# Kernel optimization log

Hardware: AMD Instinct MI355X
Metric: run time of the kernel (lower is better)

Reference implementation:

```python
import jax, jax.numpy as jnp
import numpy as np

IM_H, IM_W = 32, 32
HEADS, HEAD_DIM = 8, 32
IN_DIM = 256
OUT_DIM = 256
N = IM_H * IM_W


def _relative_indices(h, w):
    # replicate torch meshgrid('ij') + flatten logic
    gy, gx = np.meshgrid(np.arange(h), np.arange(w), indexing='ij')
    pos = np.stack([gy.reshape(-1), gx.reshape(-1)])  # (2, n)
    rel = pos[:, :, None] - pos[:, None, :]           # (2, n, n)
    r0 = (rel[0] + (h - 1)) * (2 * w - 1)
    r1 = rel[1] + (w - 1)
    return (r0 + r1).reshape(-1)                      # (n*n,)

_REL_IDX = jnp.asarray(_relative_indices(IM_H, IM_W), dtype=jnp.int32)


def setup_inputs() -> dict:
    key = jax.random.key(0)
    ks = jax.random.split(key, 8)
    d_inner = HEADS * HEAD_DIM
    x = jax.random.normal(ks[0], (16, N, IN_DIM), dtype=jnp.float32)
    Wq = jax.random.normal(ks[1], (IN_DIM, d_inner), dtype=jnp.float32) / np.sqrt(IN_DIM)
    Wk = jax.random.normal(ks[2], (IN_DIM, d_inner), dtype=jnp.float32) / np.sqrt(IN_DIM)
    Wv = jax.random.normal(ks[3], (IN_DIM, d_inner), dtype=jnp.float32) / np.sqrt(IN_DIM)
    bias_table = jax.random.normal(ks[4], ((2 * IM_H - 1) * (2 * IM_W - 1), HEADS), dtype=jnp.float32)
    Wo = jax.random.normal(ks[5], (d_inner, OUT_DIM), dtype=jnp.float32) / np.sqrt(d_inner)
    bo = jax.random.normal(ks[6], (OUT_DIM,), dtype=jnp.float32) * 0.01
    return {"x": x, "Wq": Wq, "Wk": Wk, "Wv": Wv, "bias_table": bias_table, "Wo": Wo, "bo": bo}


def reference(x, Wq, Wk, Wv, bias_table, Wo, bo):
    b, n, _ = x.shape
    scale = HEAD_DIM ** (-0.5)
    # QKV projections -> [b, h, n, d]
    def proj(W):
        return (x @ W).reshape(b, n, HEADS, HEAD_DIM).transpose(0, 2, 1, 3)
    Q, K, V = proj(Wq), proj(Wk), proj(Wv)
    # gathered relative position bias -> [1, h, n, n]
    bias = bias_table[_REL_IDX].reshape(n, n, HEADS).transpose(2, 0, 1)[None]
    scores = jnp.einsum('bhnd,bhmd->bhnm', Q, K) * scale + bias
    attn = jax.nn.softmax(scores, axis=-1)
    out = jnp.einsum('bhnm,bhmd->bhnd', attn, V)
    out = out.transpose(0, 2, 1, 3).reshape(b, n, HEADS * HEAD_DIM)
    return out @ Wo + bo  # dropout is identity in eval mode
```

## Files before the change

kernel.cpp:

```cpp
#include <hip/hip_runtime.h>


using f32x4  = __attribute__((ext_vector_type(4))) float;
using bf16x8 = __attribute__((ext_vector_type(8))) short;

__device__ __forceinline__ short f2bf(float f) {
  union { float f; unsigned u; } v; v.f = f;
  return (short)((v.u + 0x7FFFu + ((v.u >> 16) & 1u)) >> 16);
}
__device__ __forceinline__ f32x4 mfma_k32(bf16x8 a, bf16x8 b, f32x4 c) {
  return __builtin_amdgcn_mfma_f32_16x16x32_bf16(a, b, c, 0, 0, 0);
}
__device__ __forceinline__ int cvt_pk_bf16(float lo, float hi) {
  int r;
  asm("v_cvt_pk_bf16_f32 %0, %1, %2" : "=v"(r) : "v"(lo), "v"(hi));
  return r;
}
__device__ __forceinline__ f32x4 ldb(const float* __restrict__ row, int p) {
  f32x4 v;
  v[0] = row[p]; v[1] = row[p - 1]; v[2] = row[p - 2]; v[3] = row[p - 3];
  return v;
}

#define CSQ 0.25500526817f

__global__ __launch_bounds__(256) void k_prep(const float* __restrict__ Wq,
    const float* __restrict__ Wk, const float* __restrict__ Wv,
    const float* __restrict__ Wo, short* __restrict__ WT,
    const float* __restrict__ bt, float* __restrict__ Tg) {
  int bx = blockIdx.x;
  if (bx < 64) {
    __shared__ float tile[64][65];
    int wid = bx >> 4, t = bx & 15;
    int ro0 = (t & 3) * 64, co0 = (t >> 2) * 64;
    const float* W = wid == 0 ? Wq : wid == 1 ? Wk : wid == 2 ? Wv : Wo;
    int tr = threadIdx.x >> 4, tc = threadIdx.x & 15;
    #pragma unroll
    for (int c = 0; c < 4; ++c) {
      int row = c * 16 + tr;
      float4 v = *reinterpret_cast<const float4*>(
          &W[(ro0 + row) * 256 + co0 + tc * 4]);
      tile[row][tc * 4 + 0] = v.x;
      tile[row][tc * 4 + 1] = v.y;
      tile[row][tc * 4 + 2] = v.z;
      tile[row][tc * 4 + 3] = v.w;
    }
    __syncthreads();
    #pragma unroll
    for (int c = 0; c < 4; ++c) {
      int orow = c * 16 + tr;
      short4 s;
      s.x = f2bf(tile[tc * 4 + 0][orow]);
      s.y = f2bf(tile[tc * 4 + 1][orow]);
      s.z = f2bf(tile[tc * 4 + 2][orow]);
      s.w = f2bf(tile[tc * 4 + 3][orow]);
      *reinterpret_cast<short4*>(
          &WT[wid * 65536 + (co0 + orow) * 256 + ro0 + tc * 4]) = s;
    }
  } else {
    int idx = (bx - 64) * 256 + threadIdx.x;
    int h = idx >> 12, i = idx & 4095;
    if (i < 3969) Tg[idx] = bt[i * 8 + h] * 1.4426950408889634f;
  }
}

__global__ __launch_bounds__(256) void k_qkv(const float* __restrict__ x,
    const short* __restrict__ WT,
    short* __restrict__ Q, short* __restrict__ K, short* __restrict__ Vt) {
  __shared__ short Wlds[2][4096];
  char* lbase = (char*)Wlds;
  const int tid = threadIdx.x;
  const int w = tid >> 6, l = tid & 63, lr = l & 15, lg = l >> 4;
  const int m0 = blockIdx.x * 64;
  const int wi = blockIdx.y;
  const char* Wb = (const char*)(WT + wi * 65536);
  const float* xrow = x + (size_t)(m0 + w * 16 + lr) * 256;
  bf16x8 af[8];
  #pragma unroll
  for (int kc = 0; kc < 8; ++kc) {
    float4 a = *reinterpret_cast<const float4*>(xrow + kc * 32 + lg * 8);
    float4 c = *reinterpret_cast<const float4*>(xrow + kc * 32 + lg * 8 + 4);
    union { int i4[4]; bf16x8 v; } u;
    u.i4[0] = cvt_pk_bf16(a.x, a.y);
    u.i4[1] = cvt_pk_bf16(a.z, a.w);
    u.i4[2] = cvt_pk_bf16(c.x, c.y);
    u.i4[3] = cvt_pk_bf16(c.z, c.w);
    af[kc] = u.v;
  }
  const int Lb0 = tid * 16, Lb1 = 4096 + tid * 16;
  const int P0 = Lb0 ^ (((Lb0 >> 9) & 7) << 4);
  const int P1 = Lb1 ^ (((Lb1 >> 9) & 7) << 4);
  int rdo[8];
  #pragma unroll
  for (int kc = 0; kc < 8; ++kc) {
    int Lg = lr * 512 + kc * 64 + lg * 16;
    rdo[kc] = Lg ^ ((lr & 7) << 4);
  }
  {
    int4 s0 = *reinterpret_cast<const int4*>(Wb + Lb0);
    int4 s1 = *reinterpret_cast<const int4*>(Wb + Lb1);
    *reinterpret_cast<int4*>(lbase + P0) = s0;
    *reinterpret_cast<int4*>(lbase + P1) = s1;
  }
  __syncthreads();
  #pragma unroll 2
  for (int nt = 0; nt < 16; ++nt) {
    const int cur = nt & 1, nxt = cur ^ 1;
    int4 t0, t1;
    if (nt < 15) {
      t0 = *reinterpret_cast<const int4*>(Wb + (nt + 1) * 8192 + Lb0);
      t1 = *reinterpret_cast<const int4*>(Wb + (nt + 1) * 8192 + Lb1);
    }
    f32x4 acc = {0.f, 0.f, 0.f, 0.f};
    #pragma unroll
    for (int kc = 0; kc < 8; ++kc) {
      bf16x8 bfr = *reinterpret_cast<const bf16x8*>(lbase + cur * 8192 + rdo[kc]);
      acc = mfma_k32(af[kc], bfr, acc);
    }
    int colb = nt * 16 + lr;
    int h = colb >> 5, d = colb & 31;
    if (wi == 2) {
      int m = m0 + w * 16 + lg * 4;
      int b = m >> 10, n0 = m & 1023;
      int js = n0 >> 5;
      int lgv = (n0 & 15) >> 2, hi = (n0 >> 4) & 1;
      int jp = lgv * 8 + hi * 4;
      short4 vv;
      vv.x = f2bf(acc[0]); vv.y = f2bf(acc[1]);
      vv.z = f2bf(acc[2]); vv.w = f2bf(acc[3]);
      *reinterpret_cast<short4*>(
          &Vt[(((size_t)(b * 8 + h) * 32 + js) << 10) + d * 32 + jp]) = vv;
    } else {
      #pragma unroll
      for (int r = 0; r < 4; ++r) {
        int m = m0 + w * 16 + lg * 4 + r;
        int b = m >> 10, n = m & 1023;
        short val = (wi == 0) ? f2bf(acc[r] * CSQ) : f2bf(acc[r]);
        if (wi == 0)
          Q[((size_t)(b * 8 + h) * 1024 + n) * 32 + d] = val;
        else
          K[((size_t)(b * 8 + h) * 1024 + n) * 32 + d] = val;
      }
    }
    if (nt < 15) {
      *reinterpret_cast<int4*>(lbase + nxt * 8192 + P0) = t0;
      *reinterpret_cast<int4*>(lbase + nxt * 8192 + P1) = t1;
    }
    __syncthreads();
  }
}

__global__ __launch_bounds__(512) void k_attn(const short* __restrict__ Q,
    const short* __restrict__ K, const short* __restrict__ Vt,
    const float* __restrict__ Tg, short* __restrict__ aout) {
  __shared__ char smraw[24576];
  float* Tlds = (float*)smraw;
  auto mO  = (float(*)[4][4][64])smraw;
  auto mls = (float(*)[2][4][64])(smraw + 16384);
  const int tid = threadIdx.x, bid = blockIdx.x;
  const int h = bid & 7, qt = (bid >> 3) & 7, b = bid >> 6;
  const float* Th = Tg + (h << 12);
  for (int t = tid; t < 3969; t += 512) Tlds[t] = Th[t];
  __syncthreads();
  const int wg = tid >> 6, l = tid & 63, lr = l & 15, lg = l >> 4;
  const int w = wg & 3, jh = wg >> 2;
  const size_t hoff = (size_t)(b * 8 + h) << 15;
  const short* Qh = Q + hoff;
  const short* Kh = K + hoff;
  const short* Vh = Vt + hoff;
  const int ita = qt * 4 + w;
  const int i0a = ita * 16;
  const int i0b = i0a + 512;
  const int yia = ita >> 1;
  const int pbase = ((ita & 1) << 4) + lr - lg * 4 + 31;
  bf16x8 qfa = *reinterpret_cast<const bf16x8*>(&Qh[(i0a + lr) * 32 + lg * 8]);
  bf16x8 qfb = *reinterpret_cast<const bf16x8*>(&Qh[(i0b + lr) * 32 + lg * 8]);
  bf16x8 ones;
  #pragma unroll
  for (int e = 0; e < 8; ++e) ones[e] = (short)0x3F80;
  f32x4 oa0 = {0.f,0.f,0.f,0.f}, oa1 = {0.f,0.f,0.f,0.f};
  f32x4 ob0 = {0.f,0.f,0.f,0.f}, ob1 = {0.f,0.f,0.f,0.f};
  f32x4 lsa = {0.f,0.f,0.f,0.f}, lsb = {0.f,0.f,0.f,0.f};
  const int koff0 = lr * 32 + lg * 8, koff1 = (16 + lr) * 32 + lg * 8;
  const int js0 = jh * 16, jsE = js0 + 16;
  bf16x8 kf0 = *reinterpret_cast<const bf16x8*>(&Kh[(js0 << 10) + koff0]);
  bf16x8 kf1 = *reinterpret_cast<const bf16x8*>(&Kh[(js0 << 10) + koff1]);
  bf16x8 vf0 = *reinterpret_cast<const bf16x8*>(&Vh[(js0 << 10) + koff0]);
  bf16x8 vf1 = *reinterpret_cast<const bf16x8*>(&Vh[(js0 << 10) + koff1]);
  #pragma unroll 4
  for (int js = js0; js < jsE; ++js) {
    const int jn = (js + 1 < jsE) ? js + 1 : js;
    bf16x8 nkf0 = *reinterpret_cast<const bf16x8*>(&Kh[(jn << 10) + koff0]);
    bf16x8 nkf1 = *reinterpret_cast<const bf16x8*>(&Kh[(jn << 10) + koff1]);
    bf16x8 nvf0 = *reinterpret_cast<const bf16x8*>(&Vh[(jn << 10) + koff0]);
    bf16x8 nvf1 = *reinterpret_cast<const bf16x8*>(&Vh[(jn << 10) + koff1]);
    const float* TrowA = &Tlds[(yia - js + 31) * 63];
    f32x4 bA0 = ldb(TrowA, pbase);
    f32x4 bA1 = ldb(TrowA, pbase - 16);
    f32x4 bB0 = ldb(TrowA + 1008, pbase);
    f32x4 bB1 = ldb(TrowA + 1008, pbase - 16);
    f32x4 sa0 = mfma_k32(kf0, qfa, bA0);
    f32x4 sa1 = mfma_k32(kf1, qfa, bA1);
    f32x4 sb0 = mfma_k32(kf0, qfb, bB0);
    f32x4 sb1 = mfma_k32(kf1, qfb, bB1);
    float pa0[4], pa1[4], pb0[4], pb1[4];
    #pragma unroll
    for (int r = 0; r < 4; ++r) {
      pa0[r] = __builtin_amdgcn_exp2f(sa0[r]);
      pa1[r] = __builtin_amdgcn_exp2f(sa1[r]);
      pb0[r] = __builtin_amdgcn_exp2f(sb0[r]);
      pb1[r] = __builtin_amdgcn_exp2f(sb1[r]);
    }
    union { int i4[4]; bf16x8 v; } pka, pkb;
    pka.i4[0] = cvt_pk_bf16(pa0[0], pa0[1]);
    pka.i4[1] = cvt_pk_bf16(pa0[2], pa0[3]);
    pka.i4[2] = cvt_pk_bf16(pa1[0], pa1[1]);
    pka.i4[3] = cvt_pk_bf16(pa1[2], pa1[3]);
    pkb.i4[0] = cvt_pk_bf16(pb0[0], pb0[1]);
    pkb.i4[1] = cvt_pk_bf16(pb0[2], pb0[3]);
    pkb.i4[2] = cvt_pk_bf16(pb1[0], pb1[1]);
    pkb.i4[3] = cvt_pk_bf16(pb1[2], pb1[3]);
    oa0 = mfma_k32(pka.v, vf0, oa0);
    oa1 = mfma_k32(pka.v, vf1, oa1);
    lsa = mfma_k32(pka.v, ones, lsa);
    ob0 = mfma_k32(pkb.v, vf0, ob0);
    ob1 = mfma_k32(pkb.v, vf1, ob1);
    lsb = mfma_k32(pkb.v, ones, lsb);
    kf0 = nkf0; kf1 = nkf1; vf0 = nvf0; vf1 = nvf1;
  }
  __syncthreads();
  if (jh == 1) {
    #pragma unroll
    for (int r = 0; r < 4; ++r) {
      mO[w][0][r][l] = oa0[r];
      mO[w][1][r][l] = oa1[r];
      mO[w][2][r][l] = ob0[r];
      mO[w][3][r][l] = ob1[r];
      mls[w][0][r][l] = lsa[r];
      mls[w][1][r][l] = lsb[r];
    }
  }
  __syncthreads();
  if (jh == 0) {
    #pragma unroll
    for (int r = 0; r < 4; ++r) {
      oa0[r] += mO[w][0][r][l];
      oa1[r] += mO[w][1][r][l];
      ob0[r] += mO[w][2][r][l];
      ob1[r] += mO[w][3][r][l];
      lsa[r] += mls[w][0][r][l];
      lsb[r] += mls[w][1][r][l];
    }
    #pragma unroll
    for (int r = 0; r < 4; ++r) {
      float invr = 1.0f / lsa[r];
      int n = i0a + lg * 4 + r;
      size_t base = ((size_t)b << 18) + (size_t)n * 256 + h * 32;
      aout[base + lr]      = f2bf(oa0[r] * invr);
      aout[base + 16 + lr] = f2bf(oa1[r] * invr);
    }
    #pragma unroll
    for (int r = 0; r < 4; ++r) {
      float invr = 1.0f / lsb[r];
      int n = i0b + lg * 4 + r;
      size_t base = ((size_t)b << 18) + (size_t)n * 256 + h * 32;
      aout[base + lr]      = f2bf(ob0[r] * invr);
      aout[base + 16 + lr] = f2bf(ob1[r] * invr);
    }
  }
}

__global__ __launch_bounds__(256) void k_outproj(const short* __restrict__ aout,
    const short* __restrict__ WoT, const float* __restrict__ bo,
    float* __restrict__ out) {
  __shared__ short Wlds[2][4096];
  char* lbase = (char*)Wlds;
  const int tid = threadIdx.x;
  const int w = tid >> 6, l = tid & 63, lr = l & 15, lg = l >> 4;
  const int m0 = blockIdx.x * 64;
  const int nt0 = blockIdx.y * 8;
  const char* Wb = (const char*)WoT + nt0 * 8192;
  const short* arow = aout + (size_t)(m0 + w * 16 + lr) * 256;
  bf16x8 af[8];
  #pragma unroll
  for (int kc = 0; kc < 8; ++kc)
    af[kc] = *reinterpret_cast<const bf16x8*>(arow + kc * 32 + lg * 8);
  const int Lb0 = tid * 16, Lb1 = 4096 + tid * 16;
  const int P0 = Lb0 ^ (((Lb0 >> 9) & 7) << 4);
  const int P1 = Lb1 ^ (((Lb1 >> 9) & 7) << 4);
  int rdo[8];
  #pragma unroll
  for (int kc = 0; kc < 8; ++kc) {
    int Lg = lr * 512 + kc * 64 + lg * 16;
    rdo[kc] = Lg ^ ((lr & 7) << 4);
  }
  {
    int4 s0 = *reinterpret_cast<const int4*>(Wb + Lb0);
    int4 s1 = *reinterpret_cast<const int4*>(Wb + Lb1);
    *reinterpret_cast<int4*>(lbase + P0) = s0;
    *reinterpret_cast<int4*>(lbase + P1) = s1;
  }
  __syncthreads();
  #pragma unroll 2
  for (int t = 0; t < 8; ++t) {
    const int cur = t & 1, nxt = cur ^ 1;
    int4 t0, t1;
    if (t < 7) {
      t0 = *reinterpret_cast<const int4*>(Wb + (t + 1) * 8192 + Lb0);
      t1 = *reinterpret_cast<const int4*>(Wb + (t + 1) * 8192 + Lb1);
    }
    f32x4 acc = {0.f, 0.f, 0.f, 0.f};
    #pragma unroll
    for (int kc = 0; kc < 8; ++kc) {
      bf16x8 bfr = *reinterpret_cast<const bf16x8*>(lbase + cur * 8192 + rdo[kc]);
      acc = mfma_k32(af[kc], bfr, acc);
    }
    int colb = (nt0 + t) * 16 + lr;
    float bias = bo[colb];
    #pragma unroll
    for (int r = 0; r < 4; ++r) {
      int m = m0 + w * 16 + lg * 4 + r;
      out[(size_t)m * 256 + colb] = acc[r] + bias;
    }
    if (t < 7) {
      *reinterpret_cast<int4*>(lbase + nxt * 8192 + P0) = t0;
      *reinterpret_cast<int4*>(lbase + nxt * 8192 + P1) = t1;
    }
    __syncthreads();
  }
}

extern "C" void kernel_launch(void* const* d_in, const int* in_sizes, int n_in,
                              void* d_out, int out_size, void* d_ws, size_t ws_size,
                              hipStream_t stream) {
  const float* x  = (const float*)d_in[0];
  const float* Wq = (const float*)d_in[1];
  const float* Wk = (const float*)d_in[2];
  const float* Wv = (const float*)d_in[3];
  const float* bt = (const float*)d_in[4];
  const float* Wo = (const float*)d_in[5];
  const float* bo = (const float*)d_in[6];
  float* out = (float*)d_out;
  char* ws = (char*)d_ws;
  short* WT   = (short*)ws;
  short* Qs   = (short*)(ws + 512 * 1024);
  short* Ks   = Qs + 4194304;
  short* Vts  = Ks + 4194304;
  short* aout = Vts + 4194304;
  float* Tg   = (float*)(ws + 512 * 1024 + 4ull * 8388608);

  k_prep<<<192, 256, 0, stream>>>(Wq, Wk, Wv, Wo, WT, bt, Tg);
  k_qkv<<<dim3(256, 3), 256, 0, stream>>>(x, WT, Qs, Ks, Vts);
  k_attn<<<1024, 512, 0, stream>>>(Qs, Ks, Vts, Tg, aout);
  k_outproj<<<dim3(256, 2), 256, 0, stream>>>(aout, WT + 3 * 65536, bo, out);
}
```

Measured before the change: 76.78 us.

## Drop split-KV in attention; each wave processes four query tiles over all keys

The attention kernel no longer splits the key range across two wave groups that merge partial outputs and row sums through LDS. Each 256-thread block now has every wave own four 16-row query tiles and loop over all 32 key tiles. This reuses each K/V fragment load across more query tiles and removes the LDS reduction and its barriers. In exchange the grid shrinks to 512 blocks of 4 waves, which cuts resident waves per CU and doubles the serial loop length, so there is less latency hiding. The last-iteration prefetch now reads one tile past the head's buffer.

```diff
diff --git a/kernel.cpp b/kernel.cpp
--- a/kernel.cpp
+++ b/kernel.cpp
@@ -150,122 +150,85 @@
   }
 }
 
-__global__ __launch_bounds__(512) void k_attn(const short* __restrict__ Q,
+__global__ __launch_bounds__(256) void k_attn(const short* __restrict__ Q,
     const short* __restrict__ K, const short* __restrict__ Vt,
     const float* __restrict__ Tg, short* __restrict__ aout) {
-  __shared__ char smraw[24576];
-  float* Tlds = (float*)smraw;
-  auto mO  = (float(*)[4][4][64])smraw;
-  auto mls = (float(*)[2][4][64])(smraw + 16384);
+  __shared__ float Tlds[3969];
   const int tid = threadIdx.x, bid = blockIdx.x;
-  const int h = bid & 7, qt = (bid >> 3) & 7, b = bid >> 6;
+  const int h = bid & 7, qt = (bid >> 3) & 3, b = bid >> 5;
   const float* Th = Tg + (h << 12);
-  for (int t = tid; t < 3969; t += 512) Tlds[t] = Th[t];
+  for (int t = tid; t < 3969; t += 256) Tlds[t] = Th[t];
   __syncthreads();
-  const int wg = tid >> 6, l = tid & 63, lr = l & 15, lg = l >> 4;
-  const int w = wg & 3, jh = wg >> 2;
+  const int w = tid >> 6, l = tid & 63, lr = l & 15, lg = l >> 4;
   const size_t hoff = (size_t)(b * 8 + h) << 15;
   const short* Qh = Q + hoff;
   const short* Kh = K + hoff;
   const short* Vh = Vt + hoff;
-  const int ita = qt * 4 + w;
-  const int i0a = ita * 16;
-  const int i0b = i0a + 512;
-  const int yia = ita >> 1;
-  const int pbase = ((ita & 1) << 4) + lr - lg * 4 + 31;
-  bf16x8 qfa = *reinterpret_cast<const bf16x8*>(&Qh[(i0a + lr) * 32 + lg * 8]);
-  bf16x8 qfb = *reinterpret_cast<const bf16x8*>(&Qh[(i0b + lr) * 32 + lg * 8]);
+  const int it = qt * 4 + w;
+  const int i0 = it * 16;
+  const int pbase = ((it & 1) << 4) + lr - lg * 4 + 31;
+  const float* TrowB = &Tlds[((it >> 1) + 31) * 63];
+  bf16x8 qf[4];
+  #pragma unroll
+  for (int ti = 0; ti < 4; ++ti)
+    qf[ti] = *reinterpret_cast<const bf16x8*>(
+        &Qh[(i0 + 256 * ti + lr) * 32 + lg * 8]);
   bf16x8 ones;
   #pragma unroll
   for (int e = 0; e < 8; ++e) ones[e] = (short)0x3F80;
-  f32x4 oa0 = {0.f,0.f,0.f,0.f}, oa1 = {0.f,0.f,0.f,0.f};
-  f32x4 ob0 = {0.f,0.f,0.f,0.f}, ob1 = {0.f,0.f,0.f,0.f};
-  f32x4 lsa = {0.f,0.f,0.f,0.f}, lsb = {0.f,0.f,0.f,0.f};
+  f32x4 o0[4], o1[4], ls[4];
+  #pragma unroll
+  for (int ti = 0; ti < 4; ++ti) {
+    o0[ti] = f32x4{0.f, 0.f, 0.f, 0.f};
+    o1[ti] = f32x4{0.f, 0.f, 0.f, 0.f};
+    ls[ti] = f32x4{0.f, 0.f, 0.f, 0.f};
+  }
   const int koff0 = lr * 32 + lg * 8, koff1 = (16 + lr) * 32 + lg * 8;
-  const int js0 = jh * 16, jsE = js0 + 16;
-  bf16x8 kf0 = *reinterpret_cast<const bf16x8*>(&Kh[(js0 << 10) + koff0]);
-  bf16x8 kf1 = *reinterpret_cast<const bf16x8*>(&Kh[(js0 << 10) + koff1]);
-  bf16x8 vf0 = *reinterpret_cast<const bf16x8*>(&Vh[(js0 << 10) + koff0]);
-  bf16x8 vf1 = *reinterpret_cast<const bf16x8*>(&Vh[(js0 << 10) + koff1]);
-  #pragma unroll 4
-  for (int js = js0; js < jsE; ++js) {
-    const int jn = (js + 1 < jsE) ? js + 1 : js;
+  bf16x8 kf0 = *reinterpret_cast<const bf16x8*>(&Kh[koff0]);
+  bf16x8 kf1 = *reinterpret_cast<const bf16x8*>(&Kh[koff1]);
+  bf16x8 vf0 = *reinterpret_cast<const bf16x8*>(&Vh[koff0]);
+  bf16x8 vf1 = *reinterpret_cast<const bf16x8*>(&Vh[koff1]);
+  #pragma unroll 2
+  for (int js = 0; js < 32; ++js) {
+    const int jn = js + 1;
     bf16x8 nkf0 = *reinterpret_cast<const bf16x8*>(&Kh[(jn << 10) + koff0]);
     bf16x8 nkf1 = *reinterpret_cast<const bf16x8*>(&Kh[(jn << 10) + koff1]);
     bf16x8 nvf0 = *reinterpret_cast<const bf16x8*>(&Vh[(jn << 10) + koff0]);
     bf16x8 nvf1 = *reinterpret_cast<const bf16x8*>(&Vh[(jn << 10) + koff1]);
-    const float* TrowA = &Tlds[(yia - js + 31) * 63];
-    f32x4 bA0 = ldb(TrowA, pbase);
-    f32x4 bA1 = ldb(TrowA, pbase - 16);
-    f32x4 bB0 = ldb(TrowA + 1008, pbase);
-    f32x4 bB1 = ldb(TrowA + 1008, pbase - 16);
-    f32x4 sa0 = mfma_k32(kf0, qfa, bA0);
-    f32x4 sa1 = mfma_k32(kf1, qfa, bA1);
-    f32x4 sb0 = mfma_k32(kf0, qfb, bB0);
-    f32x4 sb1 = mfma_k32(kf1, qfb, bB1);
-    float pa0[4], pa1[4], pb0[4], pb1[4];
+    const float* Tr0 = TrowB - js * 63;
+    #pragma unroll
+    for (int ti = 0; ti < 4; ++ti) {
+      const float* Tr = Tr0 + ti * 504;
+      f32x4 b0 = ldb(Tr, pbase);
+      f32x4 b1 = ldb(Tr, pbase - 16);
+      f32x4 s0 = mfma_k32(kf0, qf[ti], b0);
+      f32x4 s1 = mfma_k32(kf1, qf[ti], b1);
+      float p0[4], p1[4];
+      #pragma unroll
+      for (int r = 0; r < 4; ++r) {
+        p0[r] = __builtin_amdgcn_exp2f(s0[r]);
+        p1[r] = __builtin_amdgcn_exp2f(s1[r]);
+      }
+      union { int i4[4]; bf16x8 v; } pk;
+      pk.i4[0] = cvt_pk_bf16(p0[0], p0[1]);
+      pk.i4[1] = cvt_pk_bf16(p0[2], p0[3]);
+      pk.i4[2] = cvt_pk_bf16(p1[0], p1[1]);
+      pk.i4[3] = cvt_pk_bf16(p1[2], p1[3]);
+      o0[ti] = mfma_k32(pk.v, vf0, o0[ti]);
+      o1[ti] = mfma_k32(pk.v, vf1, o1[ti]);
+      ls[ti] = mfma_k32(pk.v, ones, ls[ti]);
+    }
+    kf0 = nkf0; kf1 = nkf1; vf0 = nvf0; vf1 = nvf1;
+  }
+  #pragma unroll
+  for (int ti = 0; ti < 4; ++ti) {
     #pragma unroll
     for (int r = 0; r < 4; ++r) {
-      pa0[r] = __builtin_amdgcn_exp2f(sa0[r]);
-      pa1[r] = __builtin_amdgcn_exp2f(sa1[r]);
-      pb0[r] = __builtin_amdgcn_exp2f(sb0[r]);
-      pb1[r] = __builtin_amdgcn_exp2f(sb1[r]);
-    }
-    union { int i4[4]; bf16x8 v; } pka, pkb;
-    pka.i4[0] = cvt_pk_bf16(pa0[0], pa0[1]);
-    pka.i4[1] = cvt_pk_bf16(pa0[2], pa0[3]);
-    pka.i4[2] = cvt_pk_bf16(pa1[0], pa1[1]);
-    pka.i4[3] = cvt_pk_bf16(pa1[2], pa1[3]);
-    pkb.i4[0] = cvt_pk_bf16(pb0[0], pb0[1]);
-    pkb.i4[1] = cvt_pk_bf16(pb0[2], pb0[3]);
-    pkb.i4[2] = cvt_pk_bf16(pb1[0], pb1[1]);
-    pkb.i4[3] = cvt_pk_bf16(pb1[2], pb1[3]);
-    oa0 = mfma_k32(pka.v, vf0, oa0);
-    oa1 = mfma_k32(pka.v, vf1, oa1);
-    lsa = mfma_k32(pka.v, ones, lsa);
-    ob0 = mfma_k32(pkb.v, vf0, ob0);
-    ob1 = mfma_k32(pkb.v, vf1, ob1);
-    lsb = mfma_k32(pkb.v, ones, lsb);
-    kf0 = nkf0; kf1 = nkf1; vf0 = nvf0; vf1 = nvf1;
-  }
-  __syncthreads();
-  if (jh == 1) {
-    #pragma unroll
-    for (int r = 0; r < 4; ++r) {
-      mO[w][0][r][l] = oa0[r];
-      mO[w][1][r][l] = oa1[r];
-      mO[w][2][r][l] = ob0[r];
-      mO[w][3][r][l] = ob1[r];
-      mls[w][0][r][l] = lsa[r];
-      mls[w][1][r][l] = lsb[r];
-    }
-  }
-  __syncthreads();
-  if (jh == 0) {
-    #pragma unroll
-    for (int r = 0; r < 4; ++r) {
-      oa0[r] += mO[w][0][r][l];
-      oa1[r] += mO[w][1][r][l];
-      ob0[r] += mO[w][2][r][l];
-      ob1[r] += mO[w][3][r][l];
-      lsa[r] += mls[w][0][r][l];
-      lsb[r] += mls[w][1][r][l];
-    }
-    #pragma unroll
-    for (int r = 0; r < 4; ++r) {
-      float invr = 1.0f / lsa[r];
-      int n = i0a + lg * 4 + r;
+      float invr = 1.0f / ls[ti][r];
+      int n = i0 + 256 * ti + lg * 4 + r;
       size_t base = ((size_t)b << 18) + (size_t)n * 256 + h * 32;
-      aout[base + lr]      = f2bf(oa0[r] * invr);
-      aout[base + 16 + lr] = f2bf(oa1[r] * invr);
-    }
-    #pragma unroll
-    for (int r = 0; r < 4; ++r) {
-      float invr = 1.0f / lsb[r];
-      int n = i0b + lg * 4 + r;
-      size_t base = ((size_t)b << 18) + (size_t)n * 256 + h * 32;
-      aout[base + lr]      = f2bf(ob0[r] * invr);
-      aout[base + 16 + lr] = f2bf(ob1[r] * invr);
+      aout[base + lr]      = f2bf(o0[ti][r] * invr);
+      aout[base + 16 + lr] = f2bf(o1[ti][r] * invr);
     }
   }
 }
@@ -351,6 +314,6 @@
 
   k_prep<<<192, 256, 0, stream>>>(Wq, Wk, Wv, Wo, WT, bt, Tg);
   k_qkv<<<dim3(256, 3), 256, 0, stream>>>(x, WT, Qs, Ks, Vts);
-  k_attn<<<1024, 512, 0, stream>>>(Qs, Ks, Vts, Tg, aout);
+  k_attn<<<512, 256, 0, stream>>>(Qs, Ks, Vts, Tg, aout);
   k_outproj<<<dim3(256, 2), 256, 0, stream>>>(aout, WT + 3 * 65536, bo, out);
 }
```

New measurement: 81.58 us. +6.3%, slower.
